# Kernel tuning notes

Hardware: AMD Instinct MI355X
Metric: run time of the kernel (lower is better)

Reference implementation:

```python
import jax, jax.numpy as jnp
import numpy as np

EMB = 1024
H = 16
DH = 64


def setup_inputs() -> dict:
    key = jax.random.key(0)
    ks = jax.random.split(key, 9)
    s = 1.0 / np.sqrt(EMB)
    so = 1.0 / np.sqrt(H * DH)
    return {
        "x": jax.random.normal(ks[0], (4, 2048, EMB), dtype=jnp.float32),
        "Wq": jax.random.uniform(ks[1], (H * DH, EMB), jnp.float32, -s, s),
        "bq": jax.random.uniform(ks[2], (H * DH,), jnp.float32, -s, s),
        "Wk": jax.random.uniform(ks[3], (H * DH, EMB), jnp.float32, -s, s),
        "bk": jax.random.uniform(ks[4], (H * DH,), jnp.float32, -s, s),
        "Wv": jax.random.uniform(ks[5], (H * DH, EMB), jnp.float32, -s, s),
        "bv": jax.random.uniform(ks[6], (H * DH,), jnp.float32, -s, s),
        "Wo": jax.random.uniform(ks[7], (EMB, H * DH), jnp.float32, -so, so),
        "bo": jax.random.uniform(ks[8], (EMB,), jnp.float32, -so, so),
    }


def reference(x, Wq, bq, Wk, bk, Wv, bv, Wo, bo):
    B, S, E = x.shape
    # project and split heads: [B, H, S, Dh]
    def proj(W, b):
        return (jnp.einsum('bse,de->bsd', x, W) + b).reshape(B, S, H, DH).transpose(0, 2, 1, 3)
    q = proj(Wq, bq)
    k = proj(Wk, bk)
    v = proj(Wv, bv)
    scores = jnp.einsum('bhsd,bhtd->bhst', q / jnp.sqrt(jnp.float32(DH)), k)
    attn = jax.nn.softmax(scores, axis=-1)
    out = jnp.einsum('bhst,bhtd->bhsd', attn, v)  # [B,H,S,Dh]
    out = out.transpose(0, 2, 1, 3).reshape(B, S, H * DH)
    return jnp.einsum('bsd,ed->bse', out, Wo) + bo
```

## Files before the change

kernel.cpp:

```cpp
#include <hip/hip_runtime.h>
#include <hip/hip_bf16.h>
#include <stdint.h>

typedef __bf16 bf16x8 __attribute__((ext_vector_type(8)));
typedef float f32x4 __attribute__((ext_vector_type(4)));
typedef float f32x16 __attribute__((ext_vector_type(16)));
typedef uint32_t u32x4 __attribute__((ext_vector_type(4)));

__device__ __forceinline__ ushort f2bf(float f) {
  uint32_t u = __builtin_bit_cast(uint32_t, f);
  u += 0x7FFFu + ((u >> 16) & 1u);
  return (ushort)(u >> 16);
}

__device__ __forceinline__ uint32_t cvtpk(float lo, float hi) {
  uint32_t r;
  asm("v_cvt_pk_bf16_f32 %0, %1, %2" : "=v"(r) : "v"(lo), "v"(hi));
  return r;
}

__device__ __forceinline__ void p32swap(uint32_t& x, uint32_t& y) {
  asm("v_permlane32_swap_b32 %0, %1" : "+v"(x), "+v"(y));
}

__device__ __forceinline__ void gload16(const void* g, void* l) {
  auto gp = reinterpret_cast<const __attribute__((address_space(1))) char*>(
      reinterpret_cast<uintptr_t>(g));
  auto lp = reinterpret_cast<__attribute__((address_space(3))) char*>(
      reinterpret_cast<uintptr_t>(l));
  __builtin_amdgcn_global_load_lds(gp, lp, 16, 0, 0);
}

__device__ __forceinline__ f32x4 mfma16(bf16x8 a, bf16x8 b, f32x4 c) {
  return __builtin_amdgcn_mfma_f32_16x16x32_bf16(a, b, c, 0, 0, 0);
}
__device__ __forceinline__ f32x16 mfma32(bf16x8 a, bf16x8 b, f32x16 c) {
  return __builtin_amdgcn_mfma_f32_32x32x16_bf16(a, b, c, 0, 0, 0);
}

#define LGKM0 do { asm volatile("s_waitcnt lgkmcnt(0)" ::: "memory"); \
                   __builtin_amdgcn_sched_barrier(0); } while (0)
#define VMW(n) do { asm volatile("s_waitcnt vmcnt(" #n ")" ::: "memory"); \
                    __builtin_amdgcn_sched_barrier(0); } while (0)
#define SBAR __builtin_amdgcn_s_barrier()

__global__ void cast_kernel(const float* __restrict__ src, ushort* __restrict__ dst) {
  int i = (blockIdx.x * 256 + threadIdx.x) * 4;
  float4 v = *(const float4*)(src + i);
  ushort4 o;
  o.x = f2bf(v.x); o.y = f2bf(v.y); o.z = f2bf(v.z); o.w = f2bf(v.w);
  *(ushort4*)(dst + i) = o;
}

template <int MODE>
__global__ __launch_bounds__(512, 2) void gemm_k(
    const ushort* __restrict__ A, const ushort* __restrict__ W,
    const float* __restrict__ b0, const float* __restrict__ b1,
    const float* __restrict__ b2,
    ushort* __restrict__ qo, ushort* __restrict__ ko, ushort* __restrict__ vo,
    float* __restrict__ fo)
{
  __shared__ ushort As[3][128 * 64];
  __shared__ ushort Bs[3][256 * 64];
  const int tid = threadIdx.x;
  const int lane = tid & 63, wid = tid >> 6;
  const int wr = wid >> 2, wc = wid & 3;
  const int l15 = lane & 15, l4 = lane >> 4;

  const int wg = blockIdx.x, nwg = gridDim.x, qch = nwg >> 3;
  const int lid = (wg & 7) * qch + (wg >> 3);
  const int bx = lid >> 6, by = lid & 63;
  const int m0 = by * 128, n0 = bx * 256;

  const char* Ag = (const char*)(A + (size_t)m0 * 1024);
  const char* Wg = (const char*)(W + (size_t)n0 * 1024);

  f32x4 acc[4][4] = {};

  const int soff = tid * 16;

  auto STAGE = [&](int d, int kt) {
    const int k0b = kt * 128;
#pragma unroll
    for (int s = 0; s < 2; ++s) {
      int off = soff + s * 8192;
      int row = off >> 7, cb = off & 127;
      int sc = cb ^ ((row & 7) << 4);
      gload16(Ag + (size_t)row * 2048 + k0b + sc, (char*)As[d] + off);
    }
#pragma unroll
    for (int s = 0; s < 4; ++s) {
      int off = soff + s * 8192;
      int row = off >> 7, cb = off & 127;
      int sc = cb ^ ((row & 7) << 4);
      gload16(Wg + (size_t)row * 2048 + k0b + sc, (char*)Bs[d] + off);
    }
  };

  bf16x8 af[4][2], bfr[4][2];

  auto EXTRACT = [&](int d) {
#pragma unroll
    for (int mt = 0; mt < 4; ++mt) {
      int row = wr * 64 + mt * 16 + l15;
      int sw = (row & 7) << 4;
#pragma unroll
      for (int kk = 0; kk < 2; ++kk)
        af[mt][kk] = *(const bf16x8*)((const char*)As[d] + row * 128 +
                                      ((kk * 64 + l4 * 16) ^ sw));
    }
#pragma unroll
    for (int nt = 0; nt < 4; ++nt) {
      int row = wc * 64 + nt * 16 + l15;
      int sw = (row & 7) << 4;
#pragma unroll
      for (int kk = 0; kk < 2; ++kk)
        bfr[nt][kk] = *(const bf16x8*)((const char*)Bs[d] + row * 128 +
                                       ((kk * 64 + l4 * 16) ^ sw));
    }
  };

  auto MFMAS = [&]() {
    __builtin_amdgcn_s_setprio(1);
#pragma unroll
    for (int kk = 0; kk < 2; ++kk)
#pragma unroll
      for (int mt = 0; mt < 4; ++mt)
#pragma unroll
        for (int nt = 0; nt < 4; ++nt)
          acc[mt][nt] = mfma16(af[mt][kk], bfr[nt][kk], acc[mt][nt]);
    __builtin_amdgcn_s_setprio(0);
  };

  STAGE(0, 0);
  STAGE(1, 1);
  VMW(6); SBAR;

#pragma unroll
  for (int t = 0; t < 14; ++t) {
    STAGE((t + 2) % 3, t + 2);
    EXTRACT(t % 3);
    LGKM0;
    MFMAS();
    VMW(6);
    SBAR;
  }
  EXTRACT(2); LGKM0; MFMAS(); VMW(0); SBAR;
  EXTRACT(0); LGKM0; MFMAS();

  if (MODE == 0) {
    const int seg = n0 >> 10;
    const int nb = n0 & 1023;
    const float* bptr = (seg == 0) ? b0 : (seg == 1) ? b1 : b2;
#pragma unroll
    for (int nt = 0; nt < 4; ++nt) {
      int nl = nb + wc * 64 + nt * 16 + l15;
      int h = nl >> 6, dd = nl & 63;
      float bias = bptr[nl];
#pragma unroll
      for (int mt = 0; mt < 4; ++mt) {
        int m = m0 + wr * 64 + mt * 16 + l4 * 4;
        int b = m >> 11, s = m & 2047;
        if (seg == 2) {
          ushort4 pk;
          pk.x = f2bf(acc[mt][nt][0] + bias);
          pk.y = f2bf(acc[mt][nt][1] + bias);
          pk.z = f2bf(acc[mt][nt][2] + bias);
          pk.w = f2bf(acc[mt][nt][3] + bias);
          *(ushort4*)(vo + (size_t)((b * 16 + h) * 64 + dd) * 2048 + s) = pk;
        } else {
          ushort* dst = (seg == 0) ? qo : ko;
          float sc = (seg == 0) ? 0.18033688011112042f : 1.0f;
#pragma unroll
          for (int r = 0; r < 4; ++r)
            dst[(size_t)((b * 16 + h) * 2048 + s + r) * 64 + dd] =
                f2bf((acc[mt][nt][r] + bias) * sc);
        }
      }
    }
  } else {
#pragma unroll
    for (int nt = 0; nt < 4; ++nt) {
      int n = n0 + wc * 64 + nt * 16 + l15;
      float bias = b0[n];
#pragma unroll
      for (int mt = 0; mt < 4; ++mt) {
        int m = m0 + wr * 64 + mt * 16 + l4 * 4;
#pragma unroll
        for (int r = 0; r < 4; ++r)
          fo[(size_t)(m + r) * 1024 + n] = acc[mt][nt][r] + bias;
      }
    }
  }
}

__global__ __launch_bounds__(256, 4) void attn_k(
    const ushort* __restrict__ Q, const ushort* __restrict__ K,
    const ushort* __restrict__ V, ushort* __restrict__ O)
{
  __shared__ ushort KVs[2][8192];
  const int tid = threadIdx.x, lane = tid & 63;
  const int l31 = lane & 31, hi = lane >> 5;
  const int w = tid >> 6;
  const int bh = blockIdx.x;
  const int b = bh >> 4, h = bh & 15;
  const int q = blockIdx.y * 128 + w * 32 + l31;
  const ushort* Qh = Q + (size_t)bh * 131072;
  const ushort* Kh = K + (size_t)bh * 131072;
  const ushort* Vh = V + (size_t)bh * 131072;

  bf16x8 qf[4];
#pragma unroll
  for (int c = 0; c < 4; ++c)
    qf[c] = *(const bf16x8*)(Qh + (size_t)q * 64 + c * 16 + hi * 8);

  u32x4 onebits;
  onebits[0] = 0x3F803F80u; onebits[1] = 0x3F803F80u;
  onebits[2] = 0x3F803F80u; onebits[3] = 0x3F803F80u;
  const bf16x8 ones = __builtin_bit_cast(bf16x8, onebits);

  f32x16 oacc[2] = {};
  float lrun = 0.f;

  const int sw = (l31 & 7) << 4;
  const int loff = tid * 16;
  const int srow = loff >> 7, scolb = loff & 127;

  auto STAGE = [&](int buf, int j) {
    char* base = (char*)KVs[buf];
#pragma unroll
    for (int sh = 0; sh < 2; ++sh) {
      int row = srow + sh * 32;
      int off = loff + sh * 4096;
      int sc = scolb ^ ((row & 7) << 4);
      gload16((const char*)Kh + (size_t)j * 8192 + row * 128 + sc, base + off);
      gload16((const char*)Vh + (size_t)row * 4096 + j * 128 + sc, base + 8192 + off);
    }
  };

  STAGE(0, 0);
  __syncthreads();
  int cur = 0;

  for (int j = 0; j < 32; ++j) {
    if (j < 31) STAGE(cur ^ 1, j + 1);
    const char* Kb = (const char*)KVs[cur];
    const char* Vb = Kb + 8192;

    f32x16 sacc[2] = {};
    __builtin_amdgcn_s_setprio(1);
#pragma unroll
    for (int t = 0; t < 2; ++t)
#pragma unroll
      for (int c = 0; c < 4; ++c) {
        bf16x8 kfr = *(const bf16x8*)(Kb + (t * 32 + l31) * 128 +
                                      ((c * 32 + hi * 16) ^ sw));
        sacc[t] = mfma32(kfr, qf[c], sacc[t]);
      }
    __builtin_amdgcn_s_setprio(0);

#pragma unroll
    for (int t = 0; t < 2; ++t)
#pragma unroll
      for (int r = 0; r < 16; ++r)
        sacc[t][r] = __builtin_amdgcn_exp2f(sacc[t][r]);

    uint32_t wlo[2][4], whi[2][4];
#pragma unroll
    for (int t = 0; t < 2; ++t)
#pragma unroll
      for (int g = 0; g < 4; ++g) {
        wlo[t][g] = cvtpk(sacc[t][g * 4 + 0], sacc[t][g * 4 + 1]);
        whi[t][g] = cvtpk(sacc[t][g * 4 + 2], sacc[t][g * 4 + 3]);
      }

    bf16x8 pb[4];
#pragma unroll
    for (int c = 0; c < 4; ++c) {
      const int t = c >> 1, gb = (c & 1) * 2;
      uint32_t x0 = wlo[t][gb], y0 = wlo[t][gb + 1];
      p32swap(x0, y0);
      uint32_t x1 = whi[t][gb], y1 = whi[t][gb + 1];
      p32swap(x1, y1);
      u32x4 wv_;
      wv_[0] = x0; wv_[1] = x1; wv_[2] = y0; wv_[3] = y1;
      pb[c] = __builtin_bit_cast(bf16x8, wv_);
    }

    f32x16 ssacc = {};
    __builtin_amdgcn_s_setprio(1);
#pragma unroll
    for (int dt = 0; dt < 2; ++dt)
#pragma unroll
      for (int c = 0; c < 4; ++c) {
        bf16x8 vfr = *(const bf16x8*)(Vb + (dt * 32 + l31) * 128 +
                                      ((c * 32 + hi * 16) ^ sw));
        oacc[dt] = mfma32(vfr, pb[c], oacc[dt]);
      }
#pragma unroll
    for (int c = 0; c < 4; ++c)
      ssacc = mfma32(ones, pb[c], ssacc);
    __builtin_amdgcn_s_setprio(0);
    lrun += ssacc[0];

    __syncthreads();
    cur ^= 1;
  }

  float linv = 1.0f / lrun;
  ushort* Ob = O + (size_t)(b * 2048 + q) * 1024 + h * 64;
#pragma unroll
  for (int dt = 0; dt < 2; ++dt)
#pragma unroll
    for (int g = 0; g < 4; ++g) {
      ushort4 o4;
      o4.x = f2bf(oacc[dt][g * 4 + 0] * linv);
      o4.y = f2bf(oacc[dt][g * 4 + 1] * linv);
      o4.z = f2bf(oacc[dt][g * 4 + 2] * linv);
      o4.w = f2bf(oacc[dt][g * 4 + 3] * linv);
      *(ushort4*)(Ob + dt * 32 + g * 8 + hi * 4) = o4;
    }
}

extern "C" void kernel_launch(void* const* d_in, const int* in_sizes, int n_in,
                              void* d_out, int out_size, void* d_ws, size_t ws_size,
                              hipStream_t stream)
{
  const float* x  = (const float*)d_in[0];
  const float* Wq = (const float*)d_in[1];
  const float* bq = (const float*)d_in[2];
  const float* Wk = (const float*)d_in[3];
  const float* bk = (const float*)d_in[4];
  const float* Wv = (const float*)d_in[5];
  const float* bv = (const float*)d_in[6];
  const float* Wo = (const float*)d_in[7];
  const float* bo = (const float*)d_in[8];
  float* out = (float*)d_out;
  ushort* ws = (ushort*)d_ws;

  ushort* xb   = ws;
  ushort* wqkv = ws + 8388608;
  ushort* wo   = ws + 11534336;
  ushort* qb   = ws + 12582912;
  ushort* kb   = ws + 20971520;
  ushort* vb   = ws + 29360128;

  cast_kernel<<<8192, 256, 0, stream>>>(x, xb);
  cast_kernel<<<1024, 256, 0, stream>>>(Wq, wqkv);
  cast_kernel<<<1024, 256, 0, stream>>>(Wk, wqkv + 1048576);
  cast_kernel<<<1024, 256, 0, stream>>>(Wv, wqkv + 2097152);
  cast_kernel<<<1024, 256, 0, stream>>>(Wo, wo);

  gemm_k<0><<<768, 512, 0, stream>>>(xb, wqkv, bq, bk, bv, qb, kb, vb, nullptr);
  attn_k<<<dim3(64, 16), 256, 0, stream>>>(qb, kb, vb, xb);
  gemm_k<1><<<256, 512, 0, stream>>>(xb, wo, bo, bo, bo, nullptr, nullptr, nullptr, out);
}
```

Baseline: 178.9 us.

## Process two 32-query groups per wave in attention to reuse K/V LDS fragments

Each attention wave now handles 64 queries (two 32-row groups) instead of 32, so each K and V fragment read from LDS feeds two MFMAs. The grid is halved along the query dimension and launch bounds drop to 2 blocks per CU to make room for the doubled accumulators and Q registers. This cuts LDS reads and global K/V staging per query, at the cost of higher register pressure, lower occupancy and fewer blocks (512) to cover the GPU.

Result: faster. 173.8 us (-2.8%).

```diff
diff --git a/kernel.cpp b/kernel.cpp
--- a/kernel.cpp
+++ b/kernel.cpp
@@ -194,7 +194,7 @@
   }
 }
 
-__global__ __launch_bounds__(256, 4) void attn_k(
+__global__ __launch_bounds__(256, 2) void attn_k(
     const ushort* __restrict__ Q, const ushort* __restrict__ K,
     const ushort* __restrict__ V, ushort* __restrict__ O)
 {
@@ -204,23 +204,25 @@
   const int w = tid >> 6;
   const int bh = blockIdx.x;
   const int b = bh >> 4, h = bh & 15;
-  const int q = blockIdx.y * 128 + w * 32 + l31;
+  const int q0 = blockIdx.y * 256 + w * 64;
   const ushort* Qh = Q + (size_t)bh * 131072;
   const ushort* Kh = K + (size_t)bh * 131072;
   const ushort* Vh = V + (size_t)bh * 131072;
 
-  bf16x8 qf[4];
-#pragma unroll
-  for (int c = 0; c < 4; ++c)
-    qf[c] = *(const bf16x8*)(Qh + (size_t)q * 64 + c * 16 + hi * 8);
+  bf16x8 qf[2][4];
+#pragma unroll
+  for (int g = 0; g < 2; ++g)
+#pragma unroll
+    for (int c = 0; c < 4; ++c)
+      qf[g][c] = *(const bf16x8*)(Qh + (size_t)(q0 + g * 32 + l31) * 64 + c * 16 + hi * 8);
 
   u32x4 onebits;
   onebits[0] = 0x3F803F80u; onebits[1] = 0x3F803F80u;
   onebits[2] = 0x3F803F80u; onebits[3] = 0x3F803F80u;
   const bf16x8 ones = __builtin_bit_cast(bf16x8, onebits);
 
-  f32x16 oacc[2] = {};
-  float lrun = 0.f;
+  f32x16 oacc[2][2] = {};
+  float lrun[2] = {0.f, 0.f};
 
   const int sw = (l31 & 7) << 4;
   const int loff = tid * 16;
@@ -247,7 +249,7 @@
     const char* Kb = (const char*)KVs[cur];
     const char* Vb = Kb + 8192;
 
-    f32x16 sacc[2] = {};
+    f32x16 sacc[2][2] = {};
     __builtin_amdgcn_s_setprio(1);
 #pragma unroll
     for (int t = 0; t < 2; ++t)
@@ -255,39 +257,42 @@
       for (int c = 0; c < 4; ++c) {
         bf16x8 kfr = *(const bf16x8*)(Kb + (t * 32 + l31) * 128 +
                                       ((c * 32 + hi * 16) ^ sw));
-        sacc[t] = mfma32(kfr, qf[c], sacc[t]);
+        sacc[0][t] = mfma32(kfr, qf[0][c], sacc[0][t]);
+        sacc[1][t] = mfma32(kfr, qf[1][c], sacc[1][t]);
       }
     __builtin_amdgcn_s_setprio(0);
 
-#pragma unroll
-    for (int t = 0; t < 2; ++t)
-#pragma unroll
-      for (int r = 0; r < 16; ++r)
-        sacc[t][r] = __builtin_amdgcn_exp2f(sacc[t][r]);
-
-    uint32_t wlo[2][4], whi[2][4];
-#pragma unroll
-    for (int t = 0; t < 2; ++t)
-#pragma unroll
-      for (int g = 0; g < 4; ++g) {
-        wlo[t][g] = cvtpk(sacc[t][g * 4 + 0], sacc[t][g * 4 + 1]);
-        whi[t][g] = cvtpk(sacc[t][g * 4 + 2], sacc[t][g * 4 + 3]);
-      }
-
-    bf16x8 pb[4];
-#pragma unroll
-    for (int c = 0; c < 4; ++c) {
-      const int t = c >> 1, gb = (c & 1) * 2;
-      uint32_t x0 = wlo[t][gb], y0 = wlo[t][gb + 1];
-      p32swap(x0, y0);
-      uint32_t x1 = whi[t][gb], y1 = whi[t][gb + 1];
-      p32swap(x1, y1);
-      u32x4 wv_;
-      wv_[0] = x0; wv_[1] = x1; wv_[2] = y0; wv_[3] = y1;
-      pb[c] = __builtin_bit_cast(bf16x8, wv_);
-    }
-
-    f32x16 ssacc = {};
+    bf16x8 pb[2][4];
+#pragma unroll
+    for (int g = 0; g < 2; ++g) {
+#pragma unroll
+      for (int t = 0; t < 2; ++t)
+#pragma unroll
+        for (int r = 0; r < 16; ++r)
+          sacc[g][t][r] = __builtin_amdgcn_exp2f(sacc[g][t][r]);
+
+      uint32_t wlo[2][4], whi[2][4];
+#pragma unroll
+      for (int t = 0; t < 2; ++t)
+#pragma unroll
+        for (int gg = 0; gg < 4; ++gg) {
+          wlo[t][gg] = cvtpk(sacc[g][t][gg * 4 + 0], sacc[g][t][gg * 4 + 1]);
+          whi[t][gg] = cvtpk(sacc[g][t][gg * 4 + 2], sacc[g][t][gg * 4 + 3]);
+        }
+#pragma unroll
+      for (int c = 0; c < 4; ++c) {
+        const int t = c >> 1, gb = (c & 1) * 2;
+        uint32_t x0 = wlo[t][gb], y0 = wlo[t][gb + 1];
+        p32swap(x0, y0);
+        uint32_t x1 = whi[t][gb], y1 = whi[t][gb + 1];
+        p32swap(x1, y1);
+        u32x4 wv_;
+        wv_[0] = x0; wv_[1] = x1; wv_[2] = y0; wv_[3] = y1;
+        pb[g][c] = __builtin_bit_cast(bf16x8, wv_);
+      }
+    }
+
+    f32x16 ssacc[2] = {};
     __builtin_amdgcn_s_setprio(1);
 #pragma unroll
     for (int dt = 0; dt < 2; ++dt)
@@ -295,31 +300,38 @@
       for (int c = 0; c < 4; ++c) {
         bf16x8 vfr = *(const bf16x8*)(Vb + (dt * 32 + l31) * 128 +
                                       ((c * 32 + hi * 16) ^ sw));
-        oacc[dt] = mfma32(vfr, pb[c], oacc[dt]);
-      }
-#pragma unroll
-    for (int c = 0; c < 4; ++c)
-      ssacc = mfma32(ones, pb[c], ssacc);
+        oacc[0][dt] = mfma32(vfr, pb[0][c], oacc[0][dt]);
+        oacc[1][dt] = mfma32(vfr, pb[1][c], oacc[1][dt]);
+      }
+#pragma unroll
+    for (int c = 0; c < 4; ++c) {
+      ssacc[0] = mfma32(ones, pb[0][c], ssacc[0]);
+      ssacc[1] = mfma32(ones, pb[1][c], ssacc[1]);
+    }
     __builtin_amdgcn_s_setprio(0);
-    lrun += ssacc[0];
+    lrun[0] += ssacc[0][0];
+    lrun[1] += ssacc[1][0];
 
     __syncthreads();
     cur ^= 1;
   }
 
-  float linv = 1.0f / lrun;
-  ushort* Ob = O + (size_t)(b * 2048 + q) * 1024 + h * 64;
-#pragma unroll
-  for (int dt = 0; dt < 2; ++dt)
-#pragma unroll
-    for (int g = 0; g < 4; ++g) {
-      ushort4 o4;
-      o4.x = f2bf(oacc[dt][g * 4 + 0] * linv);
-      o4.y = f2bf(oacc[dt][g * 4 + 1] * linv);
-      o4.z = f2bf(oacc[dt][g * 4 + 2] * linv);
-      o4.w = f2bf(oacc[dt][g * 4 + 3] * linv);
-      *(ushort4*)(Ob + dt * 32 + g * 8 + hi * 4) = o4;
-    }
+#pragma unroll
+  for (int g = 0; g < 2; ++g) {
+    float linv = 1.0f / lrun[g];
+    ushort* Ob = O + (size_t)(b * 2048 + q0 + g * 32 + l31) * 1024 + h * 64;
+#pragma unroll
+    for (int dt = 0; dt < 2; ++dt)
+#pragma unroll
+      for (int gg = 0; gg < 4; ++gg) {
+        ushort4 o4;
+        o4.x = f2bf(oacc[g][dt][gg * 4 + 0] * linv);
+        o4.y = f2bf(oacc[g][dt][gg * 4 + 1] * linv);
+        o4.z = f2bf(oacc[g][dt][gg * 4 + 2] * linv);
+        o4.w = f2bf(oacc[g][dt][gg * 4 + 3] * linv);
+        *(ushort4*)(Ob + dt * 32 + gg * 8 + hi * 4) = o4;
+      }
+  }
 }
 
 extern "C" void kernel_launch(void* const* d_in, const int* in_sizes, int n_in,
@@ -352,6 +364,6 @@
   cast_kernel<<<1024, 256, 0, stream>>>(Wo, wo);
 
   gemm_k<0><<<768, 512, 0, stream>>>(xb, wqkv, bq, bk, bv, qb, kb, vb, nullptr);
-  attn_k<<<dim3(64, 16), 256, 0, stream>>>(qb, kb, vb, xb);
+  attn_k<<<dim3(64, 8), 256, 0, stream>>>(qb, kb, vb, xb);
   gemm_k<1><<<256, 512, 0, stream>>>(xb, wo, bo, bo, bo, nullptr, nullptr, nullptr, out);
 }
```
